# Optimization experiments

Measured on AMD Instinct MI355X. Metric: run time of the kernel, lower is better.

## Reference

```python
import jax, jax.numpy as jnp
import numpy as np


def setup_inputs() -> dict:
    key = jax.random.key(0)
    ks = jax.random.split(key, 7)
    B, T, I, H, O = 64, 1024, 256, 512, 256
    s_i = 1.0 / np.sqrt(I)
    s_h = 1.0 / np.sqrt(H)
    return {
        "x": jax.random.normal(ks[0], (B, T, I), dtype=jnp.float32),
        "Wi": jax.random.normal(ks[1], (H, I), dtype=jnp.float32) * s_i,
        "bi": jax.random.normal(ks[2], (H,), dtype=jnp.float32) * s_i,
        "Wh": jax.random.normal(ks[3], (H, H), dtype=jnp.float32) * s_h,
        "bh": jax.random.normal(ks[4], (H,), dtype=jnp.float32) * s_h,
        "Wo": jax.random.normal(ks[5], (O, H), dtype=jnp.float32) * s_h,
        "bo": jax.random.normal(ks[6], (O,), dtype=jnp.float32) * s_h,
    }


def reference(x, Wi, bi, Wh, bh, Wo, bo):
    # x: [B, T, I]; recurrent tanh RNN, return final linear projection [B, O]
    B, T, I = x.shape
    H = Wi.shape[0]
    # Precompute input projections for all steps at once: [T, B, H]
    xproj = jnp.einsum('bti,hi->tbh', x, Wi) + bi + bh

    def step(h, xp_t):
        h_next = jnp.tanh(xp_t + h @ Wh.T)
        return h_next, None

    h0 = jnp.zeros((B, H), dtype=x.dtype)
    h_final, _ = jax.lax.scan(step, h0, xproj)
    return h_final @ Wo.T + bo
```

## Files before the change

kernel.cpp:

```cpp
#include <hip/hip_runtime.h>
#include <math.h>

typedef unsigned long long ulong_t;
typedef unsigned int u32x4 __attribute__((ext_vector_type(4)));

#define Bsz 64
#define Tlen 1024
#define Idim 256
#define Hdim 512
#define Odim 256

#define PB  2
#define NSL 8
#define NG  (Bsz / PB)

__device__ __forceinline__ u32x4 load2_agent(const ulong_t* p) {
    u32x4 v;
    asm volatile("global_load_dwordx4 %0, %1, off sc0 sc1\n\t"
                 "s_waitcnt vmcnt(0)"
                 : "=v"(v) : "v"(p) : "memory");
    return v;
}

__global__ __launch_bounds__(256) void xproj_kernel(
        const float* __restrict__ x, const float* __restrict__ Wi,
        const float* __restrict__ bi, const float* __restrict__ bh,
        float* __restrict__ xp, int t0, int CT) {
    __shared__ float As[16][132];
    __shared__ float Bs[16][132];
    const int tid = threadIdx.x;
    const int bm = blockIdx.x, bn = blockIdx.y;
    const int tx = tid & 15, ty = tid >> 4;

    const int f0 = tid, f1 = tid + 256;
    const int ar0 = f0 >> 2, ak0 = (f0 & 3) * 4;
    const int ar1 = f1 >> 2, ak1 = (f1 & 3) * 4;
    const int m0g = bm * 128 + ar0;
    const int m1g = bm * 128 + ar1;
    const int b0 = m0g / CT, tt0 = m0g - b0 * CT;
    const int b1 = m1g / CT, tt1 = m1g - b1 * CT;
    const float* xrow0 = x + ((size_t)b0 * Tlen + t0 + tt0) * Idim;
    const float* xrow1 = x + ((size_t)b1 * Tlen + t0 + tt1) * Idim;
    const float* wrow0 = Wi + (size_t)(bn * 128 + ar0) * Idim;
    const float* wrow1 = Wi + (size_t)(bn * 128 + ar1) * Idim;

    float acc[8][8];
#pragma unroll
    for (int i = 0; i < 8; ++i)
#pragma unroll
        for (int j = 0; j < 8; ++j) acc[i][j] = 0.0f;

    for (int kk = 0; kk < Idim; kk += 16) {
        float4 av0 = *(const float4*)(xrow0 + kk + ak0);
        float4 av1 = *(const float4*)(xrow1 + kk + ak1);
        float4 bv0 = *(const float4*)(wrow0 + kk + ak0);
        float4 bv1 = *(const float4*)(wrow1 + kk + ak1);
        __syncthreads();
        As[ak0 + 0][ar0] = av0.x; As[ak0 + 1][ar0] = av0.y;
        As[ak0 + 2][ar0] = av0.z; As[ak0 + 3][ar0] = av0.w;
        As[ak1 + 0][ar1] = av1.x; As[ak1 + 1][ar1] = av1.y;
        As[ak1 + 2][ar1] = av1.z; As[ak1 + 3][ar1] = av1.w;
        Bs[ak0 + 0][ar0] = bv0.x; Bs[ak0 + 1][ar0] = bv0.y;
        Bs[ak0 + 2][ar0] = bv0.z; Bs[ak0 + 3][ar0] = bv0.w;
        Bs[ak1 + 0][ar1] = bv1.x; Bs[ak1 + 1][ar1] = bv1.y;
        Bs[ak1 + 2][ar1] = bv1.z; Bs[ak1 + 3][ar1] = bv1.w;
        __syncthreads();
#pragma unroll
        for (int k = 0; k < 16; ++k) {
            float4 a0 = *(const float4*)&As[k][tx * 4];
            float4 a1 = *(const float4*)&As[k][64 + tx * 4];
            float4 bq0 = *(const float4*)&Bs[k][ty * 4];
            float4 bq1 = *(const float4*)&Bs[k][64 + ty * 4];
            float a[8] = {a0.x, a0.y, a0.z, a0.w, a1.x, a1.y, a1.z, a1.w};
            float bb[8] = {bq0.x, bq0.y, bq0.z, bq0.w, bq1.x, bq1.y, bq1.z, bq1.w};
#pragma unroll
            for (int i = 0; i < 8; ++i)
#pragma unroll
                for (int j = 0; j < 8; ++j) acc[i][j] += a[i] * bb[j];
        }
    }

    const int n0 = bn * 128;
    float biasv[8];
#pragma unroll
    for (int j = 0; j < 8; ++j) {
        int c = (j < 4) ? (ty * 4 + j) : (64 + ty * 4 + (j - 4));
        biasv[j] = bi[n0 + c] + bh[n0 + c];
    }
#pragma unroll
    for (int i = 0; i < 8; ++i) {
        int r = (i < 4) ? (tx * 4 + i) : (64 + tx * 4 + (i - 4));
        size_t mrow = (size_t)(bm * 128 + r);
        float4 o0 = {acc[i][0] + biasv[0], acc[i][1] + biasv[1],
                     acc[i][2] + biasv[2], acc[i][3] + biasv[3]};
        float4 o1 = {acc[i][4] + biasv[4], acc[i][5] + biasv[5],
                     acc[i][6] + biasv[6], acc[i][7] + biasv[7]};
        *(float4*)(xp + mrow * Hdim + n0 + ty * 4) = o0;
        *(float4*)(xp + mrow * Hdim + n0 + 64 + ty * 4) = o1;
    }
}

__global__ __launch_bounds__(512) void scan_reg(
        const float* __restrict__ xp, const float* __restrict__ Wh,
        ulong_t* __restrict__ hglob, int t0, int CT) {
    const int wg = blockIdx.x;
    const int g = (wg & 7) + ((wg >> 6) << 3);
    const int n = (wg >> 3) & 7;
    const int colbase = n * 64;
    const int bbase = g * PB;
    const int tid = threadIdx.x;
    const int ct = tid & 15;
    const int kg = tid >> 4;

    float4 w[4][4];
#pragma unroll
    for (int cc = 0; cc < 4; ++cc) {
        const float4* src =
            (const float4*)(Wh + (size_t)(colbase + ct * 4 + cc) * Hdim + kg * 16);
#pragma unroll
        for (int i = 0; i < 4; ++i) w[cc][i] = src[i];
    }

    __shared__ float  hs[PB][Hdim];
    __shared__ float4 red4[PB][32][17];

    const int pb_ = tid >> 8;
    const int pc  = (tid & 255) * 2;
    const bool foreign = ((pc >> 6) != n);

    {
        float v0 = 0.f, v1 = 0.f;
        if (t0 != 0) {
            const ulong_t* a =
                hglob + (((size_t)(t0 & 1)) * Bsz + bbase + pb_) * Hdim + pc;
            v0 = __uint_as_float((unsigned)a[0]);
            v1 = __uint_as_float((unsigned)a[1]);
        }
        hs[pb_][pc] = v0;
        hs[pb_][pc + 1] = v1;
    }
    __syncthreads();

    const int fb = tid >> 6;
    const int fc = tid & 63;

    float xv = 0.f;
    if (tid < 128)
        xv = xp[((size_t)(bbase + fb) * CT) * Hdim + colbase + fc];

    for (int t = 0; t < CT; ++t) {
        const int st = t0 + t;
        const int nb = (st + 1) & 1;

        float4 p0 = {0.f, 0.f, 0.f, 0.f};
        float4 p1 = {0.f, 0.f, 0.f, 0.f};
#pragma unroll
        for (int i = 0; i < 4; ++i) {
            float4 h0 = *(const float4*)&hs[0][kg * 16 + i * 4];
            float4 h1 = *(const float4*)&hs[1][kg * 16 + i * 4];
            p0.x += w[0][i].x * h0.x + w[0][i].y * h0.y + w[0][i].z * h0.z + w[0][i].w * h0.w;
            p0.y += w[1][i].x * h0.x + w[1][i].y * h0.y + w[1][i].z * h0.z + w[1][i].w * h0.w;
            p0.z += w[2][i].x * h0.x + w[2][i].y * h0.y + w[2][i].z * h0.z + w[2][i].w * h0.w;
            p0.w += w[3][i].x * h0.x + w[3][i].y * h0.y + w[3][i].z * h0.z + w[3][i].w * h0.w;
            p1.x += w[0][i].x * h1.x + w[0][i].y * h1.y + w[0][i].z * h1.z + w[0][i].w * h1.w;
            p1.y += w[1][i].x * h1.x + w[1][i].y * h1.y + w[1][i].z * h1.z + w[1][i].w * h1.w;
            p1.z += w[2][i].x * h1.x + w[2][i].y * h1.y + w[2][i].z * h1.z + w[2][i].w * h1.w;
            p1.w += w[3][i].x * h1.x + w[3][i].y * h1.y + w[3][i].z * h1.z + w[3][i].w * h1.w;
        }
        red4[0][kg][ct] = p0;
        red4[1][kg][ct] = p1;
        __syncthreads();

        float xv_next = 0.f;
        if (tid < 128 && t + 1 < CT)
            xv_next = xp[((size_t)(bbase + fb) * CT + (t + 1)) * Hdim + colbase + fc];

        if (tid < 128) {
            float s = 0.f;
#pragma unroll
            for (int k = 0; k < 32; ++k)
                s += ((const float*)&red4[fb][k][0])[fc];
            float h1v = tanhf(s + xv);
            ulong_t pk = (((ulong_t)(unsigned)(st + 1)) << 32) |
                         (ulong_t)__float_as_uint(h1v);
            __hip_atomic_store(
                &hglob[((size_t)nb * Bsz + bbase + fb) * Hdim + colbase + fc],
                pk, __ATOMIC_RELAXED, __HIP_MEMORY_SCOPE_AGENT);
            hs[fb][colbase + fc] = h1v;
        }
        xv = xv_next;

        if (t + 1 < CT) {
            if (foreign) {
                const ulong_t* a =
                    hglob + ((size_t)nb * Bsz + bbase + pb_) * Hdim + pc;
                const unsigned tagexp = (unsigned)(st + 1);
                if (tid < 128) __builtin_amdgcn_s_sleep(4);
                else           __builtin_amdgcn_s_sleep(12);
                u32x4 v = load2_agent(a);
                float f0 = __uint_as_float(v.x);
                float f1 = __uint_as_float(v.z);
                bool d0 = (v.y == tagexp);
                bool d1 = (v.w == tagexp);
                while (!(d0 && d1)) {
                    if (!d0) {
                        ulong_t q = __hip_atomic_load(a, __ATOMIC_RELAXED,
                                                      __HIP_MEMORY_SCOPE_AGENT);
                        if ((unsigned)(q >> 32) == tagexp) {
                            f0 = __uint_as_float((unsigned)q); d0 = true;
                        }
                    }
                    if (!d1) {
                        ulong_t q = __hip_atomic_load(a + 1, __ATOMIC_RELAXED,
                                                      __HIP_MEMORY_SCOPE_AGENT);
                        if ((unsigned)(q >> 32) == tagexp) {
                            f1 = __uint_as_float((unsigned)q); d1 = true;
                        }
                    }
                }
                hs[pb_][pc]     = f0;
                hs[pb_][pc + 1] = f1;
            }
            __syncthreads();
        }
    }
}

__global__ __launch_bounds__(256) void out_kernel(
        const ulong_t* __restrict__ hbuf, const float* __restrict__ Wo,
        const float* __restrict__ bo, float* __restrict__ out) {
    __shared__ float hsh[Hdim];
    const int b = blockIdx.x, o = threadIdx.x;
    hsh[o]       = __uint_as_float((unsigned)hbuf[(size_t)b * Hdim + o]);
    hsh[o + 256] = __uint_as_float((unsigned)hbuf[(size_t)b * Hdim + o + 256]);
    __syncthreads();
    const float4* wrow = (const float4*)(Wo + (size_t)o * Hdim);
    const float4* h4 = (const float4*)hsh;
    float4 a4 = {0.0f, 0.0f, 0.0f, 0.0f};
#pragma unroll 4
    for (int i = 0; i < Hdim / 4; ++i) {
        float4 ww = wrow[i];
        float4 hv = h4[i];
        a4.x += ww.x * hv.x;
        a4.y += ww.y * hv.y;
        a4.z += ww.z * hv.z;
        a4.w += ww.w * hv.w;
    }
    out[b * Odim + o] = bo[o] + ((a4.x + a4.y) + (a4.z + a4.w));
}

extern "C" void kernel_launch(void* const* d_in, const int* in_sizes, int n_in,
                              void* d_out, int out_size, void* d_ws, size_t ws_size,
                              hipStream_t stream) {
    const float* x  = (const float*)d_in[0];
    const float* Wi = (const float*)d_in[1];
    const float* bi = (const float*)d_in[2];
    const float* Wh = (const float*)d_in[3];
    const float* bh = (const float*)d_in[4];
    const float* Wo = (const float*)d_in[5];
    const float* bo = (const float*)d_in[6];
    float* out = (float*)d_out;

    const size_t hbytes = 2ull * Bsz * Hdim * sizeof(ulong_t);
    int CT = Tlen;
    while (CT > 2 && (size_t)Bsz * CT * Hdim * sizeof(float) + hbytes > ws_size)
        CT >>= 1;

    float*   xp    = (float*)d_ws;
    ulong_t* hglob = (ulong_t*)((char*)d_ws + (size_t)Bsz * CT * Hdim * sizeof(float));

    for (int t0 = 0; t0 < Tlen; t0 += CT) {
        xproj_kernel<<<dim3((Bsz * CT) / 128, Hdim / 128), 256, 0, stream>>>(
            x, Wi, bi, bh, xp, t0, CT);
        scan_reg<<<dim3(NG * NSL), 512, 0, stream>>>(xp, Wh, hglob, t0, CT);
    }
    out_kernel<<<dim3(Bsz), 256, 0, stream>>>(hglob, Wo, bo, out);
}
```

Before: 2.132 ms.

## Fuse input projection into recurrent scan kernel, dropping xproj GEMM and workspace

```diff
diff --git a/kernel.cpp b/kernel.cpp
--- a/kernel.cpp
+++ b/kernel.cpp
@@ -22,87 +22,10 @@
     return v;
 }
 
-__global__ __launch_bounds__(256) void xproj_kernel(
+__global__ __launch_bounds__(512) void scan_fused(
         const float* __restrict__ x, const float* __restrict__ Wi,
-        const float* __restrict__ bi, const float* __restrict__ bh,
-        float* __restrict__ xp, int t0, int CT) {
-    __shared__ float As[16][132];
-    __shared__ float Bs[16][132];
-    const int tid = threadIdx.x;
-    const int bm = blockIdx.x, bn = blockIdx.y;
-    const int tx = tid & 15, ty = tid >> 4;
-
-    const int f0 = tid, f1 = tid + 256;
-    const int ar0 = f0 >> 2, ak0 = (f0 & 3) * 4;
-    const int ar1 = f1 >> 2, ak1 = (f1 & 3) * 4;
-    const int m0g = bm * 128 + ar0;
-    const int m1g = bm * 128 + ar1;
-    const int b0 = m0g / CT, tt0 = m0g - b0 * CT;
-    const int b1 = m1g / CT, tt1 = m1g - b1 * CT;
-    const float* xrow0 = x + ((size_t)b0 * Tlen + t0 + tt0) * Idim;
-    const float* xrow1 = x + ((size_t)b1 * Tlen + t0 + tt1) * Idim;
-    const float* wrow0 = Wi + (size_t)(bn * 128 + ar0) * Idim;
-    const float* wrow1 = Wi + (size_t)(bn * 128 + ar1) * Idim;
-
-    float acc[8][8];
-#pragma unroll
-    for (int i = 0; i < 8; ++i)
-#pragma unroll
-        for (int j = 0; j < 8; ++j) acc[i][j] = 0.0f;
-
-    for (int kk = 0; kk < Idim; kk += 16) {
-        float4 av0 = *(const float4*)(xrow0 + kk + ak0);
-        float4 av1 = *(const float4*)(xrow1 + kk + ak1);
-        float4 bv0 = *(const float4*)(wrow0 + kk + ak0);
-        float4 bv1 = *(const float4*)(wrow1 + kk + ak1);
-        __syncthreads();
-        As[ak0 + 0][ar0] = av0.x; As[ak0 + 1][ar0] = av0.y;
-        As[ak0 + 2][ar0] = av0.z; As[ak0 + 3][ar0] = av0.w;
-        As[ak1 + 0][ar1] = av1.x; As[ak1 + 1][ar1] = av1.y;
-        As[ak1 + 2][ar1] = av1.z; As[ak1 + 3][ar1] = av1.w;
-        Bs[ak0 + 0][ar0] = bv0.x; Bs[ak0 + 1][ar0] = bv0.y;
-        Bs[ak0 + 2][ar0] = bv0.z; Bs[ak0 + 3][ar0] = bv0.w;
-        Bs[ak1 + 0][ar1] = bv1.x; Bs[ak1 + 1][ar1] = bv1.y;
-        Bs[ak1 + 2][ar1] = bv1.z; Bs[ak1 + 3][ar1] = bv1.w;
-        __syncthreads();
-#pragma unroll
-        for (int k = 0; k < 16; ++k) {
-            float4 a0 = *(const float4*)&As[k][tx * 4];
-            float4 a1 = *(const float4*)&As[k][64 + tx * 4];
-            float4 bq0 = *(const float4*)&Bs[k][ty * 4];
-            float4 bq1 = *(const float4*)&Bs[k][64 + ty * 4];
-            float a[8] = {a0.x, a0.y, a0.z, a0.w, a1.x, a1.y, a1.z, a1.w};
-            float bb[8] = {bq0.x, bq0.y, bq0.z, bq0.w, bq1.x, bq1.y, bq1.z, bq1.w};
-#pragma unroll
-            for (int i = 0; i < 8; ++i)
-#pragma unroll
-                for (int j = 0; j < 8; ++j) acc[i][j] += a[i] * bb[j];
-        }
-    }
-
-    const int n0 = bn * 128;
-    float biasv[8];
-#pragma unroll
-    for (int j = 0; j < 8; ++j) {
-        int c = (j < 4) ? (ty * 4 + j) : (64 + ty * 4 + (j - 4));
-        biasv[j] = bi[n0 + c] + bh[n0 + c];
-    }
-#pragma unroll
-    for (int i = 0; i < 8; ++i) {
-        int r = (i < 4) ? (tx * 4 + i) : (64 + tx * 4 + (i - 4));
-        size_t mrow = (size_t)(bm * 128 + r);
-        float4 o0 = {acc[i][0] + biasv[0], acc[i][1] + biasv[1],
-                     acc[i][2] + biasv[2], acc[i][3] + biasv[3]};
-        float4 o1 = {acc[i][4] + biasv[4], acc[i][5] + biasv[5],
-                     acc[i][6] + biasv[6], acc[i][7] + biasv[7]};
-        *(float4*)(xp + mrow * Hdim + n0 + ty * 4) = o0;
-        *(float4*)(xp + mrow * Hdim + n0 + 64 + ty * 4) = o1;
-    }
-}
-
-__global__ __launch_bounds__(512) void scan_reg(
-        const float* __restrict__ xp, const float* __restrict__ Wh,
-        ulong_t* __restrict__ hglob, int t0, int CT) {
+        const float* __restrict__ bi, const float* __restrict__ Wh,
+        const float* __restrict__ bh, ulong_t* __restrict__ hglob) {
     const int wg = blockIdx.x;
     const int g = (wg & 7) + ((wg >> 6) << 3);
     const int n = (wg >> 3) & 7;
@@ -120,37 +43,39 @@
 #pragma unroll
         for (int i = 0; i < 4; ++i) w[cc][i] = src[i];
     }
+    float4 wi[4][2];
+#pragma unroll
+    for (int cc = 0; cc < 4; ++cc) {
+        const float4* src =
+            (const float4*)(Wi + (size_t)(colbase + ct * 4 + cc) * Idim + kg * 8);
+#pragma unroll
+        for (int i = 0; i < 2; ++i) wi[cc][i] = src[i];
+    }
 
     __shared__ float  hs[PB][Hdim];
     __shared__ float4 red4[PB][32][17];
+    __shared__ float  xs[2][PB][Idim];
 
     const int pb_ = tid >> 8;
     const int pc  = (tid & 255) * 2;
     const bool foreign = ((pc >> 6) != n);
 
-    {
-        float v0 = 0.f, v1 = 0.f;
-        if (t0 != 0) {
-            const ulong_t* a =
-                hglob + (((size_t)(t0 & 1)) * Bsz + bbase + pb_) * Hdim + pc;
-            v0 = __uint_as_float((unsigned)a[0]);
-            v1 = __uint_as_float((unsigned)a[1]);
-        }
-        hs[pb_][pc] = v0;
-        hs[pb_][pc + 1] = v1;
-    }
-    __syncthreads();
+    const int xb = tid >> 8, xk = tid & 255;
+    const float* xrow = x + ((size_t)(bbase + xb) * Tlen) * Idim + xk;
+
+    hs[pb_][pc] = 0.f;
+    hs[pb_][pc + 1] = 0.f;
+    xs[0][xb][xk] = xrow[0];
 
     const int fb = tid >> 6;
     const int fc = tid & 63;
-
-    float xv = 0.f;
-    if (tid < 128)
-        xv = xp[((size_t)(bbase + fb) * CT) * Hdim + colbase + fc];
-
-    for (int t = 0; t < CT; ++t) {
-        const int st = t0 + t;
-        const int nb = (st + 1) & 1;
+    float biasv = 0.f;
+    if (tid < 128) biasv = bi[colbase + fc] + bh[colbase + fc];
+    __syncthreads();
+
+    for (int t = 0; t < Tlen; ++t) {
+        const int par = t & 1;
+        const int nb = (t + 1) & 1;
 
         float4 p0 = {0.f, 0.f, 0.f, 0.f};
         float4 p1 = {0.f, 0.f, 0.f, 0.f};
@@ -167,34 +92,44 @@
             p1.z += w[2][i].x * h1.x + w[2][i].y * h1.y + w[2][i].z * h1.z + w[2][i].w * h1.w;
             p1.w += w[3][i].x * h1.x + w[3][i].y * h1.y + w[3][i].z * h1.z + w[3][i].w * h1.w;
         }
+#pragma unroll
+        for (int i = 0; i < 2; ++i) {
+            float4 x0 = *(const float4*)&xs[par][0][kg * 8 + i * 4];
+            float4 x1 = *(const float4*)&xs[par][1][kg * 8 + i * 4];
+            p0.x += wi[0][i].x * x0.x + wi[0][i].y * x0.y + wi[0][i].z * x0.z + wi[0][i].w * x0.w;
+            p0.y += wi[1][i].x * x0.x + wi[1][i].y * x0.y + wi[1][i].z * x0.z + wi[1][i].w * x0.w;
+            p0.z += wi[2][i].x * x0.x + wi[2][i].y * x0.y + wi[2][i].z * x0.z + wi[2][i].w * x0.w;
+            p0.w += wi[3][i].x * x0.x + wi[3][i].y * x0.y + wi[3][i].z * x0.z + wi[3][i].w * x0.w;
+            p1.x += wi[0][i].x * x1.x + wi[0][i].y * x1.y + wi[0][i].z * x1.z + wi[0][i].w * x1.w;
+            p1.y += wi[1][i].x * x1.x + wi[1][i].y * x1.y + wi[1][i].z * x1.z + wi[1][i].w * x1.w;
+            p1.z += wi[2][i].x * x1.x + wi[2][i].y * x1.y + wi[2][i].z * x1.z + wi[2][i].w * x1.w;
+            p1.w += wi[3][i].x * x1.x + wi[3][i].y * x1.y + wi[3][i].z * x1.z + wi[3][i].w * x1.w;
+        }
         red4[0][kg][ct] = p0;
         red4[1][kg][ct] = p1;
         __syncthreads();
 
-        float xv_next = 0.f;
-        if (tid < 128 && t + 1 < CT)
-            xv_next = xp[((size_t)(bbase + fb) * CT + (t + 1)) * Hdim + colbase + fc];
-
         if (tid < 128) {
-            float s = 0.f;
+            float s = biasv;
 #pragma unroll
             for (int k = 0; k < 32; ++k)
                 s += ((const float*)&red4[fb][k][0])[fc];
-            float h1v = tanhf(s + xv);
-            ulong_t pk = (((ulong_t)(unsigned)(st + 1)) << 32) |
+            float h1v = tanhf(s);
+            ulong_t pk = (((ulong_t)(unsigned)(t + 1)) << 32) |
                          (ulong_t)__float_as_uint(h1v);
             __hip_atomic_store(
                 &hglob[((size_t)nb * Bsz + bbase + fb) * Hdim + colbase + fc],
                 pk, __ATOMIC_RELAXED, __HIP_MEMORY_SCOPE_AGENT);
             hs[fb][colbase + fc] = h1v;
         }
-        xv = xv_next;
-
-        if (t + 1 < CT) {
+
+        if (t + 1 < Tlen) {
+            float xr = xrow[(size_t)(t + 1) * Idim];
+
             if (foreign) {
                 const ulong_t* a =
                     hglob + ((size_t)nb * Bsz + bbase + pb_) * Hdim + pc;
-                const unsigned tagexp = (unsigned)(st + 1);
+                const unsigned tagexp = (unsigned)(t + 1);
                 if (tid < 128) __builtin_amdgcn_s_sleep(4);
                 else           __builtin_amdgcn_s_sleep(12);
                 u32x4 v = load2_agent(a);
@@ -221,6 +156,7 @@
                 hs[pb_][pc]     = f0;
                 hs[pb_][pc + 1] = f1;
             }
+            xs[nb][xb][xk] = xr;
             __syncthreads();
         }
     }
@@ -261,18 +197,8 @@
     const float* bo = (const float*)d_in[6];
     float* out = (float*)d_out;
 
-    const size_t hbytes = 2ull * Bsz * Hdim * sizeof(ulong_t);
-    int CT = Tlen;
-    while (CT > 2 && (size_t)Bsz * CT * Hdim * sizeof(float) + hbytes > ws_size)
-        CT >>= 1;
-
-    float*   xp    = (float*)d_ws;
-    ulong_t* hglob = (ulong_t*)((char*)d_ws + (size_t)Bsz * CT * Hdim * sizeof(float));
-
-    for (int t0 = 0; t0 < Tlen; t0 += CT) {
-        xproj_kernel<<<dim3((Bsz * CT) / 128, Hdim / 128), 256, 0, stream>>>(
-            x, Wi, bi, bh, xp, t0, CT);
-        scan_reg<<<dim3(NG * NSL), 512, 0, stream>>>(xp, Wh, hglob, t0, CT);
-    }
+    ulong_t* hglob = (ulong_t*)d_ws;
+
+    scan_fused<<<dim3(NG * NSL), 512, 0, stream>>>(x, Wi, bi, Wh, bh, hglob);
     out_kernel<<<dim3(Bsz), 256, 0, stream>>>(hglob, Wo, bo, out);
 }
```

New measurement: 2.034 ms. -4.6%, faster.
